# Kernel optimization log

Hardware: AMD Instinct MI355X
Metric: run time of the kernel (lower is better)

The kernel has to match this reference:

```python
import jax, jax.numpy as jnp
import numpy as np

B, T, F, H, P = 4, 1024, 500, 128, 64


def setup_inputs() -> dict:
    key = jax.random.key(0)
    ks = jax.random.split(key, 10)
    s_gru = 1.0 / np.sqrt(H)
    s_ctx = 1.0 / np.sqrt(2 * H * P)
    s_fc = 1.0 / np.sqrt(H)
    return {
        "x": jax.random.normal(ks[0], (B, T, F), dtype=jnp.float32),
        "W_ih": jax.random.uniform(ks[1], (3 * H, F), jnp.float32, -s_gru, s_gru),
        "W_hh": jax.random.uniform(ks[2], (3 * H, H), jnp.float32, -s_gru, s_gru),
        "b_ih": jax.random.uniform(ks[3], (3 * H,), jnp.float32, -s_gru, s_gru),
        "b_hh": jax.random.uniform(ks[4], (3 * H,), jnp.float32, -s_gru, s_gru),
        "W_ctx": jax.random.uniform(ks[5], (H, 2 * H * P), jnp.float32, -s_ctx, s_ctx),
        "b_ctx": jax.random.uniform(ks[6], (H,), jnp.float32, -s_ctx, s_ctx),
        "W_fc": jax.random.uniform(ks[7], (P, H), jnp.float32, -s_fc, s_fc),
        "b_fc": jax.random.uniform(ks[8], (P,), jnp.float32, -s_fc, s_fc),
    }


def reference(x, W_ih, W_hh, b_ih, b_hh, W_ctx, b_ctx, W_fc, b_fc):
    # Original torch code never updates `hidden` inside the time loop, so every
    # GRU step runs with h = 0 (W_hh contributes only through b_hh). For a
    # 1-layer GRU, output == new state. PyTorch gate order: r, z, n.
    Bv, Tv, _ = x.shape
    Hv = W_hh.shape[1]
    Pv = W_fc.shape[0]
    gi = jnp.einsum('btf,gf->btg', x, W_ih) + b_ih          # [B,T,3H]
    gr, gz, gn = jnp.split(gi, 3, axis=-1)
    br, bz, bn = jnp.split(b_hh, 3)
    r = jax.nn.sigmoid(gr + br)
    z = jax.nn.sigmoid(gz + bz)
    n = jnp.tanh(gn + r * bn)                               # W_hh @ 0 == 0
    states = (1.0 - z) * n                                  # [B,T,H], h' = (1-z)*n + z*0
    all_states = jnp.transpose(states, (1, 0, 2))           # [T,B,H]

    # context_mat[:, :, j] at step i = concat(state_i, state_{max(i-j,0)})
    idx = jnp.clip(jnp.arange(Tv)[:, None] - jnp.arange(Pv)[None, :], 0)  # [T,P]
    gathered = all_states[idx]                              # [T,P,B,H]
    part1 = jnp.broadcast_to(all_states[:, :, :, None], (Tv, Bv, Hv, Pv))
    part2 = jnp.transpose(gathered, (0, 2, 3, 1))           # [T,B,H,P]
    # flatten matches torch .view(B, -1) of [B, 2H, P]: channel-major then proposal
    ctx_in = jnp.concatenate([part1, part2], axis=2).reshape(Tv, Bv, 2 * Hv * Pv)
    gate = jax.nn.sigmoid(jnp.einsum('tbc,hc->tbh', ctx_in, W_ctx) + b_ctx)
    gated = all_states * gate                               # output_i * ctx gate

    outs = jnp.transpose(gated, (1, 0, 2))                  # [B,T,H]
    probs = jax.nn.sigmoid(jnp.einsum('bth,ph->btp', outs, W_fc) + b_fc)
    probs = jnp.clip(probs, 0.001, 0.999)                   # [B,T,P]
    return probs, all_states
```

## Files before the change

kernel.cpp:

```cpp
#include <hip/hip_runtime.h>


typedef short bf16x8 __attribute__((ext_vector_type(8)));
typedef float f32x4 __attribute__((ext_vector_type(4)));
typedef unsigned short u16;
typedef unsigned int u32;

__device__ __forceinline__ float bf2f(u16 u) {
  union { u32 i; float f; } v; v.i = ((u32)u) << 16; return v.f;
}
__device__ __forceinline__ u16 f2bf(float f) {
  union { float f; u32 i; } v; v.f = f;
  u32 u = v.i;
  return (u16)((u + 0x7FFFu + ((u >> 16) & 1u)) >> 16);
}
__device__ __forceinline__ float sigmoidf_(float x) {
  return 1.0f / (1.0f + __expf(-x));
}

#define NWC (64*128*128)
#define NZ  (131072)

__global__ void k_prep(const float* __restrict__ W_ctx,
                       u16* __restrict__ Wc, float* __restrict__ gate_pre) {
  int g = blockIdx.x * 256 + threadIdx.x;
  if (g < NWC) {
    int p = g >> 14;
    int rem = g & 16383;
    int hp = rem >> 7;
    int h = rem & 127;
    const float* wrow = W_ctx + hp * 16384;
    float val = wrow[8192 + h * 64 + p];
    if (p == 0) {
      float s = 0.f;
      for (int q = 0; q < 64; ++q) s += wrow[h * 64 + q];
      val += s;
    }
    Wc[g] = f2bf(val);
  } else if (g < NWC + NZ) {
    int g2 = g - NWC;
    ((float4*)gate_pre)[g2] = make_float4(0.f, 0.f, 0.f, 0.f);
  }
}

__global__ __launch_bounds__(256) void k_gemm_gi(const float* __restrict__ x,
                                                 const float* __restrict__ W_ih,
                                                 u16* __restrict__ gi_bf) {
  __shared__ u16 Asm[64][136];
  __shared__ u16 Bsm[128][136];
  const int tid = threadIdx.x;
  const int r0 = blockIdx.x * 64;
  const int n0 = blockIdx.y * 128;
  const int lane = tid & 63, wave = tid >> 6;
  const int l15 = lane & 15, quad = lane >> 4;
  f32x4 acc[4][2];
  for (int i = 0; i < 4; ++i)
    for (int j = 0; j < 2; ++j) acc[i][j] = (f32x4){0.f, 0.f, 0.f, 0.f};

  for (int kb = 0; kb < 4; ++kb) {
    const int kg = kb * 128;
    const int kcols = (kb == 3) ? 29 : 32;
    __syncthreads();
    for (int rr = 0; rr < 8; ++rr) {
      int i = rr * 256 + tid;
      int m = i >> 5, cu = i & 31;
      float4 v = make_float4(0.f, 0.f, 0.f, 0.f);
      if (cu < kcols) v = *(const float4*)(x + (size_t)(r0 + m) * 500 + kg + cu * 4);
      u16* dst = &Asm[m][cu * 4];
      dst[0] = f2bf(v.x); dst[1] = f2bf(v.y); dst[2] = f2bf(v.z); dst[3] = f2bf(v.w);
    }
    for (int rr = 0; rr < 16; ++rr) {
      int i = rr * 256 + tid;
      int n = i >> 5, cu = i & 31;
      float4 v = make_float4(0.f, 0.f, 0.f, 0.f);
      if (cu < kcols) v = *(const float4*)(W_ih + (size_t)(n0 + n) * 500 + kg + cu * 4);
      u16* dst = &Bsm[n][cu * 4];
      dst[0] = f2bf(v.x); dst[1] = f2bf(v.y); dst[2] = f2bf(v.z); dst[3] = f2bf(v.w);
    }
    __syncthreads();
    for (int kk = 0; kk < 4; ++kk) {
      int kbase = kk * 32 + quad * 8;
      bf16x8 b0 = *(const bf16x8*)&Bsm[wave * 32 + l15][kbase];
      bf16x8 b1 = *(const bf16x8*)&Bsm[wave * 32 + 16 + l15][kbase];
      for (int mt = 0; mt < 4; ++mt) {
        bf16x8 a = *(const bf16x8*)&Asm[mt * 16 + l15][kbase];
        acc[mt][0] = __builtin_amdgcn_mfma_f32_16x16x32_bf16(a, b0, acc[mt][0], 0, 0, 0);
        acc[mt][1] = __builtin_amdgcn_mfma_f32_16x16x32_bf16(a, b1, acc[mt][1], 0, 0, 0);
      }
    }
  }
  for (int mt = 0; mt < 4; ++mt)
    for (int nt = 0; nt < 2; ++nt)
      for (int rg = 0; rg < 4; ++rg) {
        int m = r0 + mt * 16 + quad * 4 + rg;
        int n = n0 + wave * 32 + nt * 16 + l15;
        gi_bf[m * 384 + n] = f2bf(acc[mt][nt][rg]);
      }
}

__global__ void k_states(const u16* __restrict__ gi_bf,
                         const float* __restrict__ b_ih, const float* __restrict__ b_hh,
                         u16* __restrict__ S_bf, float* __restrict__ out_states) {
  int g = blockIdx.x * 256 + threadIdx.x;
  int r = g >> 7, h = g & 127;
  float xr = bf2f(gi_bf[r * 384 + h])       + b_ih[h]       + b_hh[h];
  float xz = bf2f(gi_bf[r * 384 + 128 + h]) + b_ih[128 + h] + b_hh[128 + h];
  float xn = bf2f(gi_bf[r * 384 + 256 + h]) + b_ih[256 + h];
  float rg = sigmoidf_(xr);
  float zg = sigmoidf_(xz);
  float n = tanhf(xn + rg * b_hh[256 + h]);
  float s = (1.f - zg) * n;
  int b = r >> 10, t = r & 1023;
  S_bf[(t * 4 + b) * 128 + h] = f2bf(s);
  out_states[(t * 4 + b) * 128 + h] = s;
}

__global__ __launch_bounds__(256) void k_gemm_ctx(const u16* __restrict__ S_bf,
                                                  const u16* __restrict__ Wc,
                                                  float* __restrict__ gate_pre) {
  __shared__ u16 Asm[64][136];
  __shared__ u16 Bsm[128][136];
  const int tid = threadIdx.x;
  const int r0 = blockIdx.x * 64;
  const int chunk = blockIdx.y;
  const int lane = tid & 63, wave = tid >> 6;
  const int l15 = lane & 15, quad = lane >> 4;
  f32x4 acc[4][2];
  for (int i = 0; i < 4; ++i)
    for (int j = 0; j < 2; ++j) acc[i][j] = (f32x4){0.f, 0.f, 0.f, 0.f};

  for (int pi = 0; pi < 8; ++pi) {
    int p = chunk * 8 + pi;
    __syncthreads();
    for (int rr = 0; rr < 4; ++rr) {
      int e = (rr * 256 + tid) * 8;
      int m = e >> 7, c = e & 127;
      int r = r0 + m;
      int t = r >> 2, b = r & 3;
      int ts = t - p; if (ts < 0) ts = 0;
      *(uint4*)&Asm[m][c] = *(const uint4*)(S_bf + (ts * 4 + b) * 128 + c);
    }
    const u16* Wp = Wc + p * 16384;
    for (int rr = 0; rr < 8; ++rr) {
      int e = (rr * 256 + tid) * 8;
      int n = e >> 7, c = e & 127;
      *(uint4*)&Bsm[n][c] = *(const uint4*)(Wp + n * 128 + c);
    }
    __syncthreads();
    for (int kk = 0; kk < 4; ++kk) {
      int kbase = kk * 32 + quad * 8;
      bf16x8 b0 = *(const bf16x8*)&Bsm[wave * 32 + l15][kbase];
      bf16x8 b1 = *(const bf16x8*)&Bsm[wave * 32 + 16 + l15][kbase];
      for (int mt = 0; mt < 4; ++mt) {
        bf16x8 a = *(const bf16x8*)&Asm[mt * 16 + l15][kbase];
        acc[mt][0] = __builtin_amdgcn_mfma_f32_16x16x32_bf16(a, b0, acc[mt][0], 0, 0, 0);
        acc[mt][1] = __builtin_amdgcn_mfma_f32_16x16x32_bf16(a, b1, acc[mt][1], 0, 0, 0);
      }
    }
  }
  for (int mt = 0; mt < 4; ++mt)
    for (int nt = 0; nt < 2; ++nt)
      for (int rg = 0; rg < 4; ++rg) {
        int m = r0 + mt * 16 + quad * 4 + rg;
        int n = wave * 32 + nt * 16 + l15;
        atomicAdd(&gate_pre[m * 128 + n], acc[mt][nt][rg]);
      }
}

__global__ __launch_bounds__(256) void k_epilogue(const float* __restrict__ gate_pre,
                                                  const u16* __restrict__ S_bf,
                                                  const float* __restrict__ b_ctx,
                                                  const float* __restrict__ W_fc,
                                                  const float* __restrict__ b_fc,
                                                  float* __restrict__ out_probs) {
  __shared__ float Wfc[64][129];
  __shared__ float gated[16][128];
  const int tid = threadIdx.x;
  const int row0 = blockIdx.x * 16;
  for (int i = tid; i < 64 * 128; i += 256)
    Wfc[i >> 7][i & 127] = W_fc[i];
  for (int it = 0; it < 8; ++it) {
    int lr = it * 2 + (tid >> 7);
    int h = tid & 127;
    int sr = row0 + lr;
    float gp = gate_pre[sr * 128 + h] + b_ctx[h];
    float gate = sigmoidf_(gp);
    gated[lr][h] = bf2f(S_bf[sr * 128 + h]) * gate;
  }
  __syncthreads();
  for (int it = 0; it < 4; ++it) {
    int o = it * 256 + tid;
    int lr = o >> 6, pp = o & 63;
    int sr = row0 + lr;
    const float* gr = gated[lr];
    const float* wr = Wfc[pp];
    float dot = 0.f;
#pragma unroll
    for (int h = 0; h < 128; ++h) dot += gr[h] * wr[h];
    float pv = sigmoidf_(dot + b_fc[pp]);
    pv = (pv > 0.001f) ? pv : 0.001f;
    pv = (pv < 0.999f) ? pv : 0.999f;
    int t = sr >> 2, b = sr & 3;
    out_probs[(b * 1024 + t) * 64 + pp] = pv;
  }
}

extern "C" void kernel_launch(void* const* d_in, const int* in_sizes, int n_in,
                              void* d_out, int out_size, void* d_ws, size_t ws_size,
                              hipStream_t stream) {
  const float* x     = (const float*)d_in[0];
  const float* W_ih  = (const float*)d_in[1];
  const float* b_ih  = (const float*)d_in[3];
  const float* b_hh  = (const float*)d_in[4];
  const float* W_ctx = (const float*)d_in[5];
  const float* b_ctx = (const float*)d_in[6];
  const float* W_fc  = (const float*)d_in[7];
  const float* b_fc  = (const float*)d_in[8];
  float* out = (float*)d_out;

  char* ws = (char*)d_ws;
  u16*   gi_bf    = (u16*)  (ws + 0);
  u16*   S_bf     = (u16*)  (ws + 3145728);
  u16*   Wc       = (u16*)  (ws + 4194304);
  float* gate_pre = (float*)(ws + 6291456);

  k_prep<<<4608, 256, 0, stream>>>(W_ctx, Wc, gate_pre);
  k_gemm_gi<<<dim3(64, 3), 256, 0, stream>>>(x, W_ih, gi_bf);
  k_states<<<2048, 256, 0, stream>>>(gi_bf, b_ih, b_hh, S_bf, out + 262144);
  k_gemm_ctx<<<dim3(64, 8), 256, 0, stream>>>(S_bf, Wc, gate_pre);
  k_epilogue<<<256, 256, 0, stream>>>(gate_pre, S_bf, b_ctx, W_fc, b_fc, out);
}
```

Measured before the change: 145.7 us.

## Pre-convert GEMM inputs to bf16, reuse shifted state tile, replace atomics with partials

The prep kernel now transposes W_ctx through shared memory for coalesced writes and also converts x and W_ih to zero-padded bf16 copies. The input GEMM reads these directly with register prefetch and uses smaller tiles for more blocks. The context GEMM loads one widened window of states once and indexes shifted rows in LDS, prefetching weights for the next step. It writes per-chunk partial sums instead of atomics, which removes the zero-init pass, and the epilogue sums the eight partials. This adds extra workspace traffic for the bf16 copies and the partial buffers.

```diff
diff --git a/kernel.cpp b/kernel.cpp
--- a/kernel.cpp
+++ b/kernel.cpp
@@ -14,88 +14,116 @@
   u32 u = v.i;
   return (u16)((u + 0x7FFFu + ((u >> 16) & 1u)) >> 16);
 }
+__device__ __forceinline__ u32 pack2(float a, float b) {
+  return (u32)f2bf(a) | ((u32)f2bf(b) << 16);
+}
 __device__ __forceinline__ float sigmoidf_(float x) {
   return 1.0f / (1.0f + __expf(-x));
 }
 
-#define NWC (64*128*128)
-#define NZ  (131072)
-
-__global__ void k_prep(const float* __restrict__ W_ctx,
-                       u16* __restrict__ Wc, float* __restrict__ gate_pre) {
-  int g = blockIdx.x * 256 + threadIdx.x;
-  if (g < NWC) {
-    int p = g >> 14;
-    int rem = g & 16383;
-    int hp = rem >> 7;
-    int h = rem & 127;
+__global__ __launch_bounds__(256) void k_prep(const float* __restrict__ W_ctx,
+                                              const float* __restrict__ x,
+                                              const float* __restrict__ W_ih,
+                                              u16* __restrict__ Wc,
+                                              u16* __restrict__ x_pad,
+                                              u16* __restrict__ W_ihp) {
+  const int tid = threadIdx.x;
+  if (blockIdx.x < 128) {
+    __shared__ float t1[128][68];
+    __shared__ float t2[128][68];
+    __shared__ float s1[128];
+    const int hp = blockIdx.x;
     const float* wrow = W_ctx + hp * 16384;
-    float val = wrow[8192 + h * 64 + p];
-    if (p == 0) {
+    for (int it = 0; it < 8; ++it) {
+      int i = it * 256 + tid;
+      int j = i * 4;
+      int h = j >> 6, q = j & 63;
+      *(float4*)&t1[h][q] = *(const float4*)(wrow + j);
+      *(float4*)&t2[h][q] = *(const float4*)(wrow + 8192 + j);
+    }
+    __syncthreads();
+    if (tid < 128) {
       float s = 0.f;
-      for (int q = 0; q < 64; ++q) s += wrow[h * 64 + q];
-      val += s;
-    }
-    Wc[g] = f2bf(val);
-  } else if (g < NWC + NZ) {
-    int g2 = g - NWC;
-    ((float4*)gate_pre)[g2] = make_float4(0.f, 0.f, 0.f, 0.f);
-  }
-}
-
-__global__ __launch_bounds__(256) void k_gemm_gi(const float* __restrict__ x,
-                                                 const float* __restrict__ W_ih,
+      for (int q = 0; q < 64; ++q) s += t1[tid][q];
+      s1[tid] = s;
+    }
+    __syncthreads();
+    for (int it = 0; it < 8; ++it) {
+      int i = it * 256 + tid;
+      int p = i >> 5, h0 = (i & 31) * 4;
+      float v0 = t2[h0 + 0][p], v1 = t2[h0 + 1][p];
+      float v2 = t2[h0 + 2][p], v3 = t2[h0 + 3][p];
+      if (p == 0) { v0 += s1[h0]; v1 += s1[h0 + 1]; v2 += s1[h0 + 2]; v3 += s1[h0 + 3]; }
+      uint2 o; o.x = pack2(v0, v1); o.y = pack2(v2, v3);
+      *(uint2*)(Wc + p * 16384 + hp * 128 + h0) = o;
+    }
+  } else {
+    int idx = (blockIdx.x - 128) * 256 + tid;
+    const float* src; u16* dst; int row, c8;
+    if (idx < 262144) { row = idx >> 6; c8 = (idx & 63) * 8; src = x;   dst = x_pad; }
+    else { idx -= 262144; row = idx >> 6; c8 = (idx & 63) * 8; src = W_ih; dst = W_ihp; }
+    float4 a = make_float4(0.f, 0.f, 0.f, 0.f), b = a;
+    if (c8 < 500)     a = *(const float4*)(src + (size_t)row * 500 + c8);
+    if (c8 + 4 < 500) b = *(const float4*)(src + (size_t)row * 500 + c8 + 4);
+    uint4 o; o.x = pack2(a.x, a.y); o.y = pack2(a.z, a.w);
+    o.z = pack2(b.x, b.y); o.w = pack2(b.z, b.w);
+    *(uint4*)(dst + (size_t)row * 512 + c8) = o;
+  }
+}
+
+__global__ __launch_bounds__(256) void k_gemm_gi(const u16* __restrict__ A,
+                                                 const u16* __restrict__ Bw,
                                                  u16* __restrict__ gi_bf) {
   __shared__ u16 Asm[64][136];
-  __shared__ u16 Bsm[128][136];
+  __shared__ u16 Bsm[64][136];
   const int tid = threadIdx.x;
   const int r0 = blockIdx.x * 64;
-  const int n0 = blockIdx.y * 128;
-  const int lane = tid & 63, wave = tid >> 6;
+  const int n0 = blockIdx.y * 64;
+  const int lane = tid & 63, w = tid >> 6;
   const int l15 = lane & 15, quad = lane >> 4;
-  f32x4 acc[4][2];
-  for (int i = 0; i < 4; ++i)
-    for (int j = 0; j < 2; ++j) acc[i][j] = (f32x4){0.f, 0.f, 0.f, 0.f};
-
+  const int srow = tid >> 4, scol = (tid & 15) * 8;
+  f32x4 acc[4];
+  for (int i = 0; i < 4; ++i) acc[i] = (f32x4){0.f, 0.f, 0.f, 0.f};
+
+  uint4 pa[4], pb[4];
+#pragma unroll
+  for (int it = 0; it < 4; ++it) {
+    pa[it] = *(const uint4*)(A + (size_t)(r0 + it * 16 + srow) * 512 + scol);
+    pb[it] = *(const uint4*)(Bw + (size_t)(n0 + it * 16 + srow) * 512 + scol);
+  }
   for (int kb = 0; kb < 4; ++kb) {
-    const int kg = kb * 128;
-    const int kcols = (kb == 3) ? 29 : 32;
+    if (kb > 0) __syncthreads();
+#pragma unroll
+    for (int it = 0; it < 4; ++it) {
+      *(uint4*)&Asm[it * 16 + srow][scol] = pa[it];
+      *(uint4*)&Bsm[it * 16 + srow][scol] = pb[it];
+    }
     __syncthreads();
-    for (int rr = 0; rr < 8; ++rr) {
-      int i = rr * 256 + tid;
-      int m = i >> 5, cu = i & 31;
-      float4 v = make_float4(0.f, 0.f, 0.f, 0.f);
-      if (cu < kcols) v = *(const float4*)(x + (size_t)(r0 + m) * 500 + kg + cu * 4);
-      u16* dst = &Asm[m][cu * 4];
-      dst[0] = f2bf(v.x); dst[1] = f2bf(v.y); dst[2] = f2bf(v.z); dst[3] = f2bf(v.w);
-    }
-    for (int rr = 0; rr < 16; ++rr) {
-      int i = rr * 256 + tid;
-      int n = i >> 5, cu = i & 31;
-      float4 v = make_float4(0.f, 0.f, 0.f, 0.f);
-      if (cu < kcols) v = *(const float4*)(W_ih + (size_t)(n0 + n) * 500 + kg + cu * 4);
-      u16* dst = &Bsm[n][cu * 4];
-      dst[0] = f2bf(v.x); dst[1] = f2bf(v.y); dst[2] = f2bf(v.z); dst[3] = f2bf(v.w);
-    }
-    __syncthreads();
+    if (kb < 3) {
+      int kg = (kb + 1) * 128;
+#pragma unroll
+      for (int it = 0; it < 4; ++it) {
+        pa[it] = *(const uint4*)(A + (size_t)(r0 + it * 16 + srow) * 512 + kg + scol);
+        pb[it] = *(const uint4*)(Bw + (size_t)(n0 + it * 16 + srow) * 512 + kg + scol);
+      }
+    }
+#pragma unroll
     for (int kk = 0; kk < 4; ++kk) {
       int kbase = kk * 32 + quad * 8;
-      bf16x8 b0 = *(const bf16x8*)&Bsm[wave * 32 + l15][kbase];
-      bf16x8 b1 = *(const bf16x8*)&Bsm[wave * 32 + 16 + l15][kbase];
+      bf16x8 bf = *(const bf16x8*)&Bsm[w * 16 + l15][kbase];
+#pragma unroll
       for (int mt = 0; mt < 4; ++mt) {
-        bf16x8 a = *(const bf16x8*)&Asm[mt * 16 + l15][kbase];
-        acc[mt][0] = __builtin_amdgcn_mfma_f32_16x16x32_bf16(a, b0, acc[mt][0], 0, 0, 0);
-        acc[mt][1] = __builtin_amdgcn_mfma_f32_16x16x32_bf16(a, b1, acc[mt][1], 0, 0, 0);
+        bf16x8 af = *(const bf16x8*)&Asm[mt * 16 + l15][kbase];
+        acc[mt] = __builtin_amdgcn_mfma_f32_16x16x32_bf16(af, bf, acc[mt], 0, 0, 0);
       }
     }
   }
   for (int mt = 0; mt < 4; ++mt)
-    for (int nt = 0; nt < 2; ++nt)
-      for (int rg = 0; rg < 4; ++rg) {
-        int m = r0 + mt * 16 + quad * 4 + rg;
-        int n = n0 + wave * 32 + nt * 16 + l15;
-        gi_bf[m * 384 + n] = f2bf(acc[mt][nt][rg]);
-      }
+    for (int rg = 0; rg < 4; ++rg) {
+      int m = r0 + mt * 16 + quad * 4 + rg;
+      int n = n0 + w * 16 + l15;
+      gi_bf[m * 384 + n] = f2bf(acc[mt][rg]);
+    }
 }
 
 __global__ void k_states(const u16* __restrict__ gi_bf,
@@ -117,86 +145,114 @@
 
 __global__ __launch_bounds__(256) void k_gemm_ctx(const u16* __restrict__ S_bf,
                                                   const u16* __restrict__ Wc,
-                                                  float* __restrict__ gate_pre) {
-  __shared__ u16 Asm[64][136];
+                                                  float* __restrict__ partial) {
+  __shared__ u16 Asm[96][136];
   __shared__ u16 Bsm[128][136];
   const int tid = threadIdx.x;
   const int r0 = blockIdx.x * 64;
-  const int chunk = blockIdx.y;
-  const int lane = tid & 63, wave = tid >> 6;
+  const int P0 = blockIdx.y * 8;
+  const int t0 = r0 >> 2;
+  int tlo = t0 - P0 - 7; if (tlo < 0) tlo = 0;
+  const int lane = tid & 63, w = tid >> 6;
   const int l15 = lane & 15, quad = lane >> 4;
+  const int srow = tid >> 4, scol = (tid & 15) * 8;
   f32x4 acc[4][2];
   for (int i = 0; i < 4; ++i)
     for (int j = 0; j < 2; ++j) acc[i][j] = (f32x4){0.f, 0.f, 0.f, 0.f};
 
+  uint4 pa[6];
+#pragma unroll
+  for (int it = 0; it < 6; ++it) {
+    int row = it * 16 + srow;
+    int ti = tlo + (row >> 2); if (ti > 1023) ti = 1023;
+    int gr = ti * 4 + (row & 3);
+    pa[it] = *(const uint4*)(S_bf + (size_t)gr * 128 + scol);
+  }
+  uint4 pb[8];
+#pragma unroll
+  for (int it = 0; it < 8; ++it)
+    pb[it] = *(const uint4*)(Wc + (size_t)P0 * 16384 + (it * 16 + srow) * 128 + scol);
+#pragma unroll
+  for (int it = 0; it < 6; ++it) *(uint4*)&Asm[it * 16 + srow][scol] = pa[it];
+#pragma unroll
+  for (int it = 0; it < 8; ++it) *(uint4*)&Bsm[it * 16 + srow][scol] = pb[it];
+  __syncthreads();
+
   for (int pi = 0; pi < 8; ++pi) {
-    int p = chunk * 8 + pi;
-    __syncthreads();
-    for (int rr = 0; rr < 4; ++rr) {
-      int e = (rr * 256 + tid) * 8;
-      int m = e >> 7, c = e & 127;
-      int r = r0 + m;
-      int t = r >> 2, b = r & 3;
-      int ts = t - p; if (ts < 0) ts = 0;
-      *(uint4*)&Asm[m][c] = *(const uint4*)(S_bf + (ts * 4 + b) * 128 + c);
-    }
-    const u16* Wp = Wc + p * 16384;
-    for (int rr = 0; rr < 8; ++rr) {
-      int e = (rr * 256 + tid) * 8;
-      int n = e >> 7, c = e & 127;
-      *(uint4*)&Bsm[n][c] = *(const uint4*)(Wp + n * 128 + c);
-    }
-    __syncthreads();
+    int p = P0 + pi;
+    if (pi < 7) {
+#pragma unroll
+      for (int it = 0; it < 8; ++it)
+        pb[it] = *(const uint4*)(Wc + (size_t)(p + 1) * 16384 + (it * 16 + srow) * 128 + scol);
+    }
+    int lrow[4];
+#pragma unroll
+    for (int mt = 0; mt < 4; ++mt) {
+      int rA = r0 + mt * 16 + l15;
+      int tp = (rA >> 2) - p; if (tp < 0) tp = 0;
+      lrow[mt] = (tp - tlo) * 4 + (rA & 3);
+    }
+#pragma unroll
     for (int kk = 0; kk < 4; ++kk) {
       int kbase = kk * 32 + quad * 8;
-      bf16x8 b0 = *(const bf16x8*)&Bsm[wave * 32 + l15][kbase];
-      bf16x8 b1 = *(const bf16x8*)&Bsm[wave * 32 + 16 + l15][kbase];
+      bf16x8 b0 = *(const bf16x8*)&Bsm[w * 32 + l15][kbase];
+      bf16x8 b1 = *(const bf16x8*)&Bsm[w * 32 + 16 + l15][kbase];
+#pragma unroll
       for (int mt = 0; mt < 4; ++mt) {
-        bf16x8 a = *(const bf16x8*)&Asm[mt * 16 + l15][kbase];
-        acc[mt][0] = __builtin_amdgcn_mfma_f32_16x16x32_bf16(a, b0, acc[mt][0], 0, 0, 0);
-        acc[mt][1] = __builtin_amdgcn_mfma_f32_16x16x32_bf16(a, b1, acc[mt][1], 0, 0, 0);
-      }
-    }
-  }
+        bf16x8 af = *(const bf16x8*)&Asm[lrow[mt]][kbase];
+        acc[mt][0] = __builtin_amdgcn_mfma_f32_16x16x32_bf16(af, b0, acc[mt][0], 0, 0, 0);
+        acc[mt][1] = __builtin_amdgcn_mfma_f32_16x16x32_bf16(af, b1, acc[mt][1], 0, 0, 0);
+      }
+    }
+    if (pi < 7) {
+      __syncthreads();
+#pragma unroll
+      for (int it = 0; it < 8; ++it) *(uint4*)&Bsm[it * 16 + srow][scol] = pb[it];
+      __syncthreads();
+    }
+  }
+  float* outp = partial + (size_t)blockIdx.y * (4096 * 128);
   for (int mt = 0; mt < 4; ++mt)
     for (int nt = 0; nt < 2; ++nt)
       for (int rg = 0; rg < 4; ++rg) {
         int m = r0 + mt * 16 + quad * 4 + rg;
-        int n = wave * 32 + nt * 16 + l15;
-        atomicAdd(&gate_pre[m * 128 + n], acc[mt][nt][rg]);
-      }
-}
-
-__global__ __launch_bounds__(256) void k_epilogue(const float* __restrict__ gate_pre,
-                                                  const u16* __restrict__ S_bf,
+        int n = w * 32 + nt * 16 + l15;
+        outp[m * 128 + n] = acc[mt][nt][rg];
+      }
+}
+
+__global__ __launch_bounds__(256) void k_epilogue(const float* __restrict__ partial,
+                                                  const float* __restrict__ states,
                                                   const float* __restrict__ b_ctx,
                                                   const float* __restrict__ W_fc,
                                                   const float* __restrict__ b_fc,
                                                   float* __restrict__ out_probs) {
-  __shared__ float Wfc[64][129];
-  __shared__ float gated[16][128];
-  const int tid = threadIdx.x;
-  const int row0 = blockIdx.x * 16;
-  for (int i = tid; i < 64 * 128; i += 256)
-    Wfc[i >> 7][i & 127] = W_fc[i];
-  for (int it = 0; it < 8; ++it) {
-    int lr = it * 2 + (tid >> 7);
-    int h = tid & 127;
+  __shared__ float WfcT[128][68];
+  __shared__ float gated[8][128];
+  const int tid = threadIdx.x;
+  const int row0 = blockIdx.x * 8;
+  for (int it = 0; it < 32; ++it) {
+    int i = it * 256 + tid;
+    int pp = i >> 7, h = i & 127;
+    WfcT[h][pp] = W_fc[i];
+  }
+  for (int it = 0; it < 4; ++it) {
+    int i = it * 256 + tid;
+    int lr = i >> 7, h = i & 127;
     int sr = row0 + lr;
-    float gp = gate_pre[sr * 128 + h] + b_ctx[h];
-    float gate = sigmoidf_(gp);
-    gated[lr][h] = bf2f(S_bf[sr * 128 + h]) * gate;
+    float gp = b_ctx[h];
+#pragma unroll
+    for (int c = 0; c < 8; ++c) gp += partial[(size_t)c * (4096 * 128) + sr * 128 + h];
+    gated[lr][h] = states[sr * 128 + h] * sigmoidf_(gp);
   }
   __syncthreads();
-  for (int it = 0; it < 4; ++it) {
+  for (int it = 0; it < 2; ++it) {
     int o = it * 256 + tid;
     int lr = o >> 6, pp = o & 63;
     int sr = row0 + lr;
-    const float* gr = gated[lr];
-    const float* wr = Wfc[pp];
     float dot = 0.f;
 #pragma unroll
-    for (int h = 0; h < 128; ++h) dot += gr[h] * wr[h];
+    for (int h = 0; h < 128; ++h) dot += gated[lr][h] * WfcT[h][pp];
     float pv = sigmoidf_(dot + b_fc[pp]);
     pv = (pv > 0.001f) ? pv : 0.001f;
     pv = (pv < 0.999f) ? pv : 0.999f;
@@ -219,14 +275,16 @@
   float* out = (float*)d_out;
 
   char* ws = (char*)d_ws;
-  u16*   gi_bf    = (u16*)  (ws + 0);
-  u16*   S_bf     = (u16*)  (ws + 3145728);
-  u16*   Wc       = (u16*)  (ws + 4194304);
-  float* gate_pre = (float*)(ws + 6291456);
-
-  k_prep<<<4608, 256, 0, stream>>>(W_ctx, Wc, gate_pre);
-  k_gemm_gi<<<dim3(64, 3), 256, 0, stream>>>(x, W_ih, gi_bf);
+  u16*   x_pad   = (u16*)  (ws + 0);
+  u16*   W_ihp   = (u16*)  (ws + 4194304);
+  u16*   gi_bf   = (u16*)  (ws + 4587520);
+  u16*   S_bf    = (u16*)  (ws + 7733248);
+  u16*   Wc      = (u16*)  (ws + 8781824);
+  float* partial = (float*)(ws + 10878976);
+
+  k_prep<<<1248, 256, 0, stream>>>(W_ctx, x, W_ih, Wc, x_pad, W_ihp);
+  k_gemm_gi<<<dim3(64, 6), 256, 0, stream>>>(x_pad, W_ihp, gi_bf);
   k_states<<<2048, 256, 0, stream>>>(gi_bf, b_ih, b_hh, S_bf, out + 262144);
-  k_gemm_ctx<<<dim3(64, 8), 256, 0, stream>>>(S_bf, Wc, gate_pre);
-  k_epilogue<<<256, 256, 0, stream>>>(gate_pre, S_bf, b_ctx, W_fc, b_fc, out);
-}
+  k_gemm_ctx<<<dim3(64, 8), 256, 0, stream>>>(S_bf, Wc, partial);
+  k_epilogue<<<512, 256, 0, stream>>>(partial, out + 262144, b_ctx, W_fc, b_fc, out);
+}
```

New measurement: 153.1 us. +5.1%, slower.
